# Kernel optimization log

Hardware: AMD Instinct MI355X
Metric: run time of the kernel (lower is better)

The kernel has to match this reference:

```python
import jax, jax.numpy as jnp
import numpy as np

# NaiveMatryoshkaLinear(dim=4096, hidden_dim=4096, heads=[8,8,16], bias=False)
# head_dim = 4096 // 32 = 128
# input_dims  (cumsum heads * head_dim) = [1024, 2048, 4096]
# output_dims (heads * head_dim)        = [1024, 1024, 2048]
INPUT_DIMS = (1024, 2048, 4096)
OUTPUT_DIMS = (1024, 1024, 2048)


def setup_inputs() -> dict:
    key = jax.random.key(0)
    kx, k0, k1, k2 = jax.random.split(key, 4)
    x = jax.random.normal(kx, (4, 4096, 4096), dtype=jnp.float32)
    # torch nn.Linear weight layout: (out_features, in_features), kaiming-uniform-ish init
    def init_w(k, out_d, in_d):
        bound = 1.0 / np.sqrt(in_d)
        return jax.random.uniform(k, (out_d, in_d), dtype=jnp.float32, minval=-bound, maxval=bound)
    W0 = init_w(k0, OUTPUT_DIMS[0], INPUT_DIMS[0])
    W1 = init_w(k1, OUTPUT_DIMS[1], INPUT_DIMS[1])
    W2 = init_w(k2, OUTPUT_DIMS[2], INPUT_DIMS[2])
    return {"x": x, "W0": W0, "W1": W1, "W2": W2}


def reference(x, W0, W1, W2):
    # Block-triangular matryoshka linear: each head i projects the prefix
    # x[..., :input_dims[i]] with its own weight, outputs are concatenated.
    y0 = jnp.einsum('bsd,od->bso', x[..., :INPUT_DIMS[0]], W0)
    y1 = jnp.einsum('bsd,od->bso', x[..., :INPUT_DIMS[1]], W1)
    y2 = jnp.einsum('bsd,od->bso', x[..., :INPUT_DIMS[2]], W2)
    return jnp.concatenate([y0, y1, y2], axis=-1)  # [4, 4096, 4096]
```

## Files before the change

### kernel.cpp

```cpp
#include <hip/hip_runtime.h>
#include <hip/hip_bf16.h>


typedef short bf16x8 __attribute__((ext_vector_type(8)));
typedef float f32x4 __attribute__((ext_vector_type(4)));

__device__ __forceinline__ ushort f2bf(float f) {
  union { float f; unsigned u; } c; c.f = f;
  unsigned u = c.u;
  unsigned r = u + 0x7fffu + ((u >> 16) & 1u);
  return (ushort)(r >> 16);
}

__global__ void cvt_f32_bf16(const float* __restrict__ in,
                             ushort* __restrict__ out, int n4) {
  int i = blockIdx.x * blockDim.x + threadIdx.x;
  int stride = gridDim.x * blockDim.x;
  const float4* in4 = (const float4*)in;
  ushort4* out4 = (ushort4*)out;
  for (int j = i; j < n4; j += stride) {
    float4 v = in4[j];
    ushort4 o;
    o.x = f2bf(v.x); o.y = f2bf(v.y); o.z = f2bf(v.z); o.w = f2bf(v.w);
    out4[j] = o;
  }
}

__device__ __forceinline__ void gload16(const ushort* g, const ushort* l) {
  __builtin_amdgcn_global_load_lds(
      (const __attribute__((address_space(1))) void*)g,
      (__attribute__((address_space(3))) void*)l, 16, 0, 0);
}

#define TILE_E 8192

#define MF(av, bv, mi, ni) \
  acc[mi][ni] = __builtin_amdgcn_mfma_f32_16x16x32_bf16(av, bv, acc[mi][ni], 0, 0, 0)

__global__ __launch_bounds__(512, 2) void matry_gemm(
    const ushort* __restrict__ xbf,
    const ushort* __restrict__ w0,
    const ushort* __restrict__ w1,
    const ushort* __restrict__ w2,
    float* __restrict__ out) {
  __shared__ __align__(16) ushort sA[4][TILE_E];
  __shared__ __align__(16) ushort sB[4][TILE_E];

  const int bid = blockIdx.x;
  const int rt = bid & 63;
  const int ct = bid >> 6;

  int K; const ushort* W; int nl0;
  if (ct < 4)      { K = 1024; W = w0; nl0 = ct * 256; }
  else if (ct < 8) { K = 2048; W = w1; nl0 = (ct - 4) * 256; }
  else             { K = 4096; W = w2; nl0 = (ct - 8) * 256; }
  const int NT = K >> 5;
  const int m0 = rt * 256;
  const int n0 = ct * 256;

  const int tid  = threadIdx.x;
  const int wid  = tid >> 6;
  const int lane = tid & 63;
  const int wm = wid >> 2;
  const int wn = wid & 3;
  const int fr = lane & 15;
  const int swz_e = (((lane >> 4) ^ (lane & 3)) << 3);

  const int srow = tid >> 2;
  const int scol = (((tid & 3) ^ (srow & 3)) << 3);
  const ushort* Asrc0 = xbf + (size_t)(m0 + srow) * 4096 + scol;
  const ushort* Asrc1 = Asrc0 + (size_t)128 * 4096;
  const ushort* Bsrc0 = W + (size_t)(nl0 + srow) * K + scol;
  const ushort* Bsrc1 = Bsrc0 + (size_t)128 * K;
  const int d0 = tid * 8;
  const int d1 = 4096 + tid * 8;

  f32x4 acc[8][4];
#pragma unroll
  for (int mi = 0; mi < 8; ++mi)
#pragma unroll
    for (int ni = 0; ni < 4; ++ni)
      acc[mi][ni] = (f32x4){0.f, 0.f, 0.f, 0.f};

#pragma unroll
  for (int pt = 0; pt < 3; ++pt) {
    const int ks = pt * 32;
    gload16(Asrc0 + ks, &sA[pt][d0]);
    gload16(Asrc1 + ks, &sA[pt][d1]);
    gload16(Bsrc0 + ks, &sB[pt][d0]);
    gload16(Bsrc1 + ks, &sB[pt][d1]);
  }
  asm volatile("s_waitcnt vmcnt(8)" ::: "memory");
  __builtin_amdgcn_s_barrier();

  for (int t = 0; t < NT; ++t) {
    const int b = t & 3;
    const ushort* pa = &sA[b][(wm * 128 + fr) * 32 + swz_e];
    const ushort* pb = &sB[b][(wn * 64 + fr) * 32 + swz_e];
    const int ts = (t + 3 < NT) ? (t + 3) : (NT - 1);
    const int ks = ts << 5;
    const int bs = (t + 3) & 3;

    bf16x8 a0 = *(const bf16x8*)(pa);
    bf16x8 a1 = *(const bf16x8*)(pa + 512);
    bf16x8 a2 = *(const bf16x8*)(pa + 1024);
    bf16x8 a3 = *(const bf16x8*)(pa + 1536);
    bf16x8 b0 = *(const bf16x8*)(pb);
    bf16x8 b1 = *(const bf16x8*)(pb + 512);
    bf16x8 b2 = *(const bf16x8*)(pb + 1024);
    bf16x8 b3 = *(const bf16x8*)(pb + 1536);
    gload16(Asrc0 + ks, &sA[bs][d0]);
    gload16(Asrc1 + ks, &sA[bs][d1]);
    __builtin_amdgcn_s_setprio(1);
    MF(a0, b0, 0, 0); MF(a0, b1, 0, 1); MF(a0, b2, 0, 2); MF(a0, b3, 0, 3);
    MF(a1, b0, 1, 0); MF(a1, b1, 1, 1); MF(a1, b2, 1, 2); MF(a1, b3, 1, 3);
    MF(a2, b0, 2, 0); MF(a2, b1, 2, 1); MF(a2, b2, 2, 2); MF(a2, b3, 2, 3);
    MF(a3, b0, 3, 0); MF(a3, b1, 3, 1); MF(a3, b2, 3, 2); MF(a3, b3, 3, 3);
    __builtin_amdgcn_s_setprio(0);

    bf16x8 a4 = *(const bf16x8*)(pa + 2048);
    bf16x8 a5 = *(const bf16x8*)(pa + 2560);
    bf16x8 a6 = *(const bf16x8*)(pa + 3072);
    bf16x8 a7 = *(const bf16x8*)(pa + 3584);
    gload16(Bsrc0 + ks, &sB[bs][d0]);
    gload16(Bsrc1 + ks, &sB[bs][d1]);
    __builtin_amdgcn_s_setprio(1);
    MF(a4, b0, 4, 0); MF(a4, b1, 4, 1); MF(a4, b2, 4, 2); MF(a4, b3, 4, 3);
    MF(a5, b0, 5, 0); MF(a5, b1, 5, 1); MF(a5, b2, 5, 2); MF(a5, b3, 5, 3);
    MF(a6, b0, 6, 0); MF(a6, b1, 6, 1); MF(a6, b2, 6, 2); MF(a6, b3, 6, 3);
    MF(a7, b0, 7, 0); MF(a7, b1, 7, 1); MF(a7, b2, 7, 2); MF(a7, b3, 7, 3);
    __builtin_amdgcn_s_setprio(0);

    asm volatile("s_waitcnt vmcnt(8)" ::: "memory");
    __builtin_amdgcn_s_barrier();
  }

  const int rq = (lane >> 4) * 4;
#pragma unroll
  for (int mi = 0; mi < 8; ++mi) {
#pragma unroll
    for (int ni = 0; ni < 4; ++ni) {
      const int n = n0 + wn * 64 + ni * 16 + fr;
#pragma unroll
      for (int r = 0; r < 4; ++r) {
        const int m = m0 + wm * 128 + mi * 16 + rq + r;
        out[(size_t)m * 4096 + n] = acc[mi][ni][r];
      }
    }
  }
}

__global__ void naive_kernel(const float* __restrict__ x,
                             const float* __restrict__ W0,
                             const float* __restrict__ W1,
                             const float* __restrict__ W2,
                             float* __restrict__ out) {
  long idx = (long)blockIdx.x * 256 + threadIdx.x;
  int n = (int)(idx & 4095);
  long m = idx >> 12;
  int K; const float* W; int nl;
  if (n < 1024)      { K = 1024; W = W0; nl = n; }
  else if (n < 2048) { K = 2048; W = W1; nl = n - 1024; }
  else               { K = 4096; W = W2; nl = n - 2048; }
  const float* xr = x + m * 4096;
  const float* wr = W + (long)nl * K;
  float s = 0.f;
  for (int k = 0; k < K; ++k) s += xr[k] * wr[k];
  out[idx] = s;
}

extern "C" void kernel_launch(void* const* d_in, const int* in_sizes, int n_in,
                              void* d_out, int out_size, void* d_ws,
                              size_t ws_size, hipStream_t stream) {
  const float* x  = (const float*)d_in[0];
  const float* W0 = (const float*)d_in[1];
  const float* W1 = (const float*)d_in[2];
  const float* W2 = (const float*)d_in[3];
  float* out = (float*)d_out;

  const size_t xN  = (size_t)16384 * 4096;
  const size_t w0N = (size_t)1024 * 1024;
  const size_t w1N = (size_t)1024 * 2048;
  const size_t w2N = (size_t)2048 * 4096;
  const size_t need = (xN + w0N + w1N + w2N) * sizeof(ushort);

  if (ws_size >= need) {
    ushort* xbf = (ushort*)d_ws;
    ushort* w0b = xbf + xN;
    ushort* w1b = w0b + w0N;
    ushort* w2b = w1b + w1N;
    cvt_f32_bf16<<<2048, 256, 0, stream>>>(x, xbf, (int)(xN >> 2));
    cvt_f32_bf16<<<256, 256, 0, stream>>>(W0, w0b, (int)(w0N >> 2));
    cvt_f32_bf16<<<256, 256, 0, stream>>>(W1, w1b, (int)(w1N >> 2));
    cvt_f32_bf16<<<512, 256, 0, stream>>>(W2, w2b, (int)(w2N >> 2));
    matry_gemm<<<1024, 512, 0, stream>>>(xbf, w0b, w1b, w2b, out);
  } else {
    naive_kernel<<<(int)((xN + 255) / 256), 256, 0, stream>>>(x, W0, W1, W2, out);
  }
}
```

Baseline: 462.9 us.

## Prepack weights into MFMA fragment layout and load B directly to registers

Weights are now converted into a fragment-ordered bf16 layout in one fused conversion kernel, so each wave can load its B operands straight from global memory into registers instead of staging them through LDS. This halves shared memory use, which may allow more occupancy, and removes the LDS reads for B. The main loop is unrolled by two with ping-pong B register buffers, and the LDS swizzle is changed. The risk is global-load latency for B sitting on the critical path, since it is prefetched only one step ahead, and heavier register use.

```diff
diff --git a/kernel.cpp b/kernel.cpp
--- a/kernel.cpp
+++ b/kernel.cpp
@@ -12,8 +12,8 @@
   return (ushort)(r >> 16);
 }
 
-__global__ void cvt_f32_bf16(const float* __restrict__ in,
-                             ushort* __restrict__ out, int n4) {
+__global__ void cvt_x_bf16(const float* __restrict__ in,
+                           ushort* __restrict__ out, int n4) {
   int i = blockIdx.x * blockDim.x + threadIdx.x;
   int stride = gridDim.x * blockDim.x;
   const float4* in4 = (const float4*)in;
@@ -26,34 +26,60 @@
   }
 }
 
+__global__ void cvt_w_frag(const float* __restrict__ W0,
+                           const float* __restrict__ W1,
+                           const float* __restrict__ W2,
+                           ushort* __restrict__ w0f,
+                           ushort* __restrict__ w1f,
+                           ushort* __restrict__ w2f) {
+  const int T0 = 131072;
+  const int T1 = T0 + 262144;
+  const int T2 = T1 + 1048576;
+  int i = blockIdx.x * blockDim.x + threadIdx.x;
+  int stride = gridDim.x * blockDim.x;
+  for (int j = i; j < T2; j += stride) {
+    const float* W; ushort* Wf; int K, n, k8;
+    if (j < T0)      { W = W0; Wf = w0f; K = 1024; n = j >> 7;         k8 = j & 127; }
+    else if (j < T1) { W = W1; Wf = w1f; K = 2048; n = (j - T0) >> 8;  k8 = (j - T0) & 255; }
+    else             { W = W2; Wf = w2f; K = 4096; n = (j - T1) >> 9;  k8 = (j - T1) & 511; }
+    const int kb = k8 >> 2, hi = k8 & 3, nb = n >> 4, nl = n & 15;
+    const size_t dst = ((size_t)(nb * (K >> 5) + kb) << 9) + (((hi << 4) | nl) << 3);
+    const float4* s = (const float4*)(W + (size_t)n * K + (k8 << 3));
+    float4 v0 = s[0], v1 = s[1];
+    bf16x8 o;
+    o[0] = (short)f2bf(v0.x); o[1] = (short)f2bf(v0.y);
+    o[2] = (short)f2bf(v0.z); o[3] = (short)f2bf(v0.w);
+    o[4] = (short)f2bf(v1.x); o[5] = (short)f2bf(v1.y);
+    o[6] = (short)f2bf(v1.z); o[7] = (short)f2bf(v1.w);
+    *(bf16x8*)(Wf + dst) = o;
+  }
+}
+
 __device__ __forceinline__ void gload16(const ushort* g, const ushort* l) {
   __builtin_amdgcn_global_load_lds(
       (const __attribute__((address_space(1))) void*)g,
       (__attribute__((address_space(3))) void*)l, 16, 0, 0);
 }
 
-#define TILE_E 8192
-
 #define MF(av, bv, mi, ni) \
   acc[mi][ni] = __builtin_amdgcn_mfma_f32_16x16x32_bf16(av, bv, acc[mi][ni], 0, 0, 0)
 
 __global__ __launch_bounds__(512, 2) void matry_gemm(
     const ushort* __restrict__ xbf,
-    const ushort* __restrict__ w0,
-    const ushort* __restrict__ w1,
-    const ushort* __restrict__ w2,
+    const ushort* __restrict__ w0f,
+    const ushort* __restrict__ w1f,
+    const ushort* __restrict__ w2f,
     float* __restrict__ out) {
-  __shared__ __align__(16) ushort sA[4][TILE_E];
-  __shared__ __align__(16) ushort sB[4][TILE_E];
+  __shared__ __align__(16) ushort sA[4][8192];
 
   const int bid = blockIdx.x;
   const int rt = bid & 63;
   const int ct = bid >> 6;
 
-  int K; const ushort* W; int nl0;
-  if (ct < 4)      { K = 1024; W = w0; nl0 = ct * 256; }
-  else if (ct < 8) { K = 2048; W = w1; nl0 = (ct - 4) * 256; }
-  else             { K = 4096; W = w2; nl0 = (ct - 8) * 256; }
+  int K; const ushort* Wf; int nl0;
+  if (ct < 4)      { K = 1024; Wf = w0f; nl0 = ct * 256; }
+  else if (ct < 8) { K = 2048; Wf = w1f; nl0 = (ct - 4) * 256; }
+  else             { K = 4096; Wf = w2f; nl0 = (ct - 8) * 256; }
   const int NT = K >> 5;
   const int m0 = rt * 256;
   const int n0 = ct * 256;
@@ -64,17 +90,17 @@
   const int wm = wid >> 2;
   const int wn = wid & 3;
   const int fr = lane & 15;
-  const int swz_e = (((lane >> 4) ^ (lane & 3)) << 3);
+  const int swz_e = (((lane >> 4) ^ ((lane >> 1) & 3)) << 3);
 
   const int srow = tid >> 2;
-  const int scol = (((tid & 3) ^ (srow & 3)) << 3);
+  const int scol = (((tid & 3) ^ ((tid >> 3) & 3)) << 3);
   const ushort* Asrc0 = xbf + (size_t)(m0 + srow) * 4096 + scol;
   const ushort* Asrc1 = Asrc0 + (size_t)128 * 4096;
-  const ushort* Bsrc0 = W + (size_t)(nl0 + srow) * K + scol;
-  const ushort* Bsrc1 = Bsrc0 + (size_t)128 * K;
   const int d0 = tid * 8;
   const int d1 = 4096 + tid * 8;
 
+  const ushort* Bfw = Wf + (((size_t)((nl0 >> 4) + wn * 4) * NT) << 9) + lane * 8;
+
   f32x4 acc[8][4];
 #pragma unroll
   for (int mi = 0; mi < 8; ++mi)
@@ -84,55 +110,78 @@
 
 #pragma unroll
   for (int pt = 0; pt < 3; ++pt) {
-    const int ks = pt * 32;
-    gload16(Asrc0 + ks, &sA[pt][d0]);
-    gload16(Asrc1 + ks, &sA[pt][d1]);
-    gload16(Bsrc0 + ks, &sB[pt][d0]);
-    gload16(Bsrc1 + ks, &sB[pt][d1]);
-  }
+    gload16(Asrc0 + pt * 32, &sA[pt][d0]);
+    gload16(Asrc1 + pt * 32, &sA[pt][d1]);
+  }
+  bf16x8 bE[4], bO[4];
+#pragma unroll
+  for (int ni = 0; ni < 4; ++ni)
+    bE[ni] = *(const bf16x8*)(Bfw + ((size_t)(ni * NT) << 9));
   asm volatile("s_waitcnt vmcnt(8)" ::: "memory");
   __builtin_amdgcn_s_barrier();
 
-  for (int t = 0; t < NT; ++t) {
-    const int b = t & 3;
-    const ushort* pa = &sA[b][(wm * 128 + fr) * 32 + swz_e];
-    const ushort* pb = &sB[b][(wn * 64 + fr) * 32 + swz_e];
-    const int ts = (t + 3 < NT) ? (t + 3) : (NT - 1);
-    const int ks = ts << 5;
-    const int bs = (t + 3) & 3;
-
-    bf16x8 a0 = *(const bf16x8*)(pa);
-    bf16x8 a1 = *(const bf16x8*)(pa + 512);
-    bf16x8 a2 = *(const bf16x8*)(pa + 1024);
-    bf16x8 a3 = *(const bf16x8*)(pa + 1536);
-    bf16x8 b0 = *(const bf16x8*)(pb);
-    bf16x8 b1 = *(const bf16x8*)(pb + 512);
-    bf16x8 b2 = *(const bf16x8*)(pb + 1024);
-    bf16x8 b3 = *(const bf16x8*)(pb + 1536);
-    gload16(Asrc0 + ks, &sA[bs][d0]);
-    gload16(Asrc1 + ks, &sA[bs][d1]);
-    __builtin_amdgcn_s_setprio(1);
-    MF(a0, b0, 0, 0); MF(a0, b1, 0, 1); MF(a0, b2, 0, 2); MF(a0, b3, 0, 3);
-    MF(a1, b0, 1, 0); MF(a1, b1, 1, 1); MF(a1, b2, 1, 2); MF(a1, b3, 1, 3);
-    MF(a2, b0, 2, 0); MF(a2, b1, 2, 1); MF(a2, b2, 2, 2); MF(a2, b3, 2, 3);
-    MF(a3, b0, 3, 0); MF(a3, b1, 3, 1); MF(a3, b2, 3, 2); MF(a3, b3, 3, 3);
-    __builtin_amdgcn_s_setprio(0);
-
-    bf16x8 a4 = *(const bf16x8*)(pa + 2048);
-    bf16x8 a5 = *(const bf16x8*)(pa + 2560);
-    bf16x8 a6 = *(const bf16x8*)(pa + 3072);
-    bf16x8 a7 = *(const bf16x8*)(pa + 3584);
-    gload16(Bsrc0 + ks, &sB[bs][d0]);
-    gload16(Bsrc1 + ks, &sB[bs][d1]);
-    __builtin_amdgcn_s_setprio(1);
-    MF(a4, b0, 4, 0); MF(a4, b1, 4, 1); MF(a4, b2, 4, 2); MF(a4, b3, 4, 3);
-    MF(a5, b0, 5, 0); MF(a5, b1, 5, 1); MF(a5, b2, 5, 2); MF(a5, b3, 5, 3);
-    MF(a6, b0, 6, 0); MF(a6, b1, 6, 1); MF(a6, b2, 6, 2); MF(a6, b3, 6, 3);
-    MF(a7, b0, 7, 0); MF(a7, b1, 7, 1); MF(a7, b2, 7, 2); MF(a7, b3, 7, 3);
-    __builtin_amdgcn_s_setprio(0);
-
-    asm volatile("s_waitcnt vmcnt(8)" ::: "memory");
-    __builtin_amdgcn_s_barrier();
+  for (int t = 0; t < NT; t += 2) {
+    {
+      const ushort* pa = &sA[t & 3][(wm * 128 + fr) * 32 + swz_e];
+      bf16x8 a0 = *(const bf16x8*)(pa);
+      bf16x8 a1 = *(const bf16x8*)(pa + 512);
+      bf16x8 a2 = *(const bf16x8*)(pa + 1024);
+      bf16x8 a3 = *(const bf16x8*)(pa + 1536);
+      bf16x8 a4 = *(const bf16x8*)(pa + 2048);
+      bf16x8 a5 = *(const bf16x8*)(pa + 2560);
+      bf16x8 a6 = *(const bf16x8*)(pa + 3072);
+      bf16x8 a7 = *(const bf16x8*)(pa + 3584);
+      const int ts = (t + 3 < NT) ? (t + 3) : (NT - 1);
+      const int bs = (t + 3) & 3;
+      gload16(Asrc0 + (ts << 5), &sA[bs][d0]);
+      gload16(Asrc1 + (ts << 5), &sA[bs][d1]);
+#pragma unroll
+      for (int ni = 0; ni < 4; ++ni)
+        bO[ni] = *(const bf16x8*)(Bfw + ((size_t)(ni * NT + t + 1) << 9));
+      __builtin_amdgcn_s_setprio(1);
+      MF(a0, bE[0], 0, 0); MF(a0, bE[1], 0, 1); MF(a0, bE[2], 0, 2); MF(a0, bE[3], 0, 3);
+      MF(a1, bE[0], 1, 0); MF(a1, bE[1], 1, 1); MF(a1, bE[2], 1, 2); MF(a1, bE[3], 1, 3);
+      MF(a2, bE[0], 2, 0); MF(a2, bE[1], 2, 1); MF(a2, bE[2], 2, 2); MF(a2, bE[3], 2, 3);
+      MF(a3, bE[0], 3, 0); MF(a3, bE[1], 3, 1); MF(a3, bE[2], 3, 2); MF(a3, bE[3], 3, 3);
+      MF(a4, bE[0], 4, 0); MF(a4, bE[1], 4, 1); MF(a4, bE[2], 4, 2); MF(a4, bE[3], 4, 3);
+      MF(a5, bE[0], 5, 0); MF(a5, bE[1], 5, 1); MF(a5, bE[2], 5, 2); MF(a5, bE[3], 5, 3);
+      MF(a6, bE[0], 6, 0); MF(a6, bE[1], 6, 1); MF(a6, bE[2], 6, 2); MF(a6, bE[3], 6, 3);
+      MF(a7, bE[0], 7, 0); MF(a7, bE[1], 7, 1); MF(a7, bE[2], 7, 2); MF(a7, bE[3], 7, 3);
+      __builtin_amdgcn_s_setprio(0);
+      asm volatile("s_waitcnt vmcnt(16)" ::: "memory");
+      __builtin_amdgcn_s_barrier();
+    }
+    {
+      const ushort* pa = &sA[(t + 1) & 3][(wm * 128 + fr) * 32 + swz_e];
+      bf16x8 a0 = *(const bf16x8*)(pa);
+      bf16x8 a1 = *(const bf16x8*)(pa + 512);
+      bf16x8 a2 = *(const bf16x8*)(pa + 1024);
+      bf16x8 a3 = *(const bf16x8*)(pa + 1536);
+      bf16x8 a4 = *(const bf16x8*)(pa + 2048);
+      bf16x8 a5 = *(const bf16x8*)(pa + 2560);
+      bf16x8 a6 = *(const bf16x8*)(pa + 3072);
+      bf16x8 a7 = *(const bf16x8*)(pa + 3584);
+      const int ts = (t + 4 < NT) ? (t + 4) : (NT - 1);
+      const int bs = (t + 4) & 3;
+      gload16(Asrc0 + (ts << 5), &sA[bs][d0]);
+      gload16(Asrc1 + (ts << 5), &sA[bs][d1]);
+      const int tl = (t + 2 < NT) ? (t + 2) : (NT - 1);
+#pragma unroll
+      for (int ni = 0; ni < 4; ++ni)
+        bE[ni] = *(const bf16x8*)(Bfw + ((size_t)(ni * NT + tl) << 9));
+      __builtin_amdgcn_s_setprio(1);
+      MF(a0, bO[0], 0, 0); MF(a0, bO[1], 0, 1); MF(a0, bO[2], 0, 2); MF(a0, bO[3], 0, 3);
+      MF(a1, bO[0], 1, 0); MF(a1, bO[1], 1, 1); MF(a1, bO[2], 1, 2); MF(a1, bO[3], 1, 3);
+      MF(a2, bO[0], 2, 0); MF(a2, bO[1], 2, 1); MF(a2, bO[2], 2, 2); MF(a2, bO[3], 2, 3);
+      MF(a3, bO[0], 3, 0); MF(a3, bO[1], 3, 1); MF(a3, bO[2], 3, 2); MF(a3, bO[3], 3, 3);
+      MF(a4, bO[0], 4, 0); MF(a4, bO[1], 4, 1); MF(a4, bO[2], 4, 2); MF(a4, bO[3], 4, 3);
+      MF(a5, bO[0], 5, 0); MF(a5, bO[1], 5, 1); MF(a5, bO[2], 5, 2); MF(a5, bO[3], 5, 3);
+      MF(a6, bO[0], 6, 0); MF(a6, bO[1], 6, 1); MF(a6, bO[2], 6, 2); MF(a6, bO[3], 6, 3);
+      MF(a7, bO[0], 7, 0); MF(a7, bO[1], 7, 1); MF(a7, bO[2], 7, 2); MF(a7, bO[3], 7, 3);
+      __builtin_amdgcn_s_setprio(0);
+      asm volatile("s_waitcnt vmcnt(16)" ::: "memory");
+      __builtin_amdgcn_s_barrier();
+    }
   }
 
   const int rq = (lane >> 4) * 4;
@@ -186,14 +235,12 @@
 
   if (ws_size >= need) {
     ushort* xbf = (ushort*)d_ws;
-    ushort* w0b = xbf + xN;
-    ushort* w1b = w0b + w0N;
-    ushort* w2b = w1b + w1N;
-    cvt_f32_bf16<<<2048, 256, 0, stream>>>(x, xbf, (int)(xN >> 2));
-    cvt_f32_bf16<<<256, 256, 0, stream>>>(W0, w0b, (int)(w0N >> 2));
-    cvt_f32_bf16<<<256, 256, 0, stream>>>(W1, w1b, (int)(w1N >> 2));
-    cvt_f32_bf16<<<512, 256, 0, stream>>>(W2, w2b, (int)(w2N >> 2));
-    matry_gemm<<<1024, 512, 0, stream>>>(xbf, w0b, w1b, w2b, out);
+    ushort* w0f = xbf + xN;
+    ushort* w1f = w0f + w0N;
+    ushort* w2f = w1f + w1N;
+    cvt_x_bf16<<<2048, 256, 0, stream>>>(x, xbf, (int)(xN >> 2));
+    cvt_w_frag<<<2048, 256, 0, stream>>>(W0, W1, W2, w0f, w1f, w2f);
+    matry_gemm<<<1024, 512, 0, stream>>>(xbf, w0f, w1f, w2f, out);
   } else {
     naive_kernel<<<(int)((xN + 255) / 256), 256, 0, stream>>>(x, W0, W1, W2, out);
   }
```

After: 502.1 us. 8.5% more time.
